# Optimization experiments

Measured on AMD Instinct MI355X. Metric: run time of the kernel, lower is better.

The kernel has to match this reference:

```python
import jax, jax.numpy as jnp
import numpy as np
import math

IN_C = 768
CA = 384
K1 = (3, 1, 1)
K2 = (1, 3, 3)
K3 = (3, 3, 3)


def _dwconv3d(x, w, b):
    # x: [B, Ca, T, H, W]; w: [Ca, 1, kt, kh, kw]; depthwise (groups = Ca)
    pads = [(k // 2, k // 2) for k in w.shape[2:]]
    y = jax.lax.conv_general_dilated(
        x, w, window_strides=(1, 1, 1), padding=pads,
        feature_group_count=x.shape[1],
        dimension_numbers=("NCDHW", "OIDHW", "NCDHW"))
    return y + b[None, :, None, None, None]


def setup_inputs() -> dict:
    key = jax.random.key(0)
    ks = jax.random.split(key, 12)
    s = 0.02
    x = jax.random.normal(ks[0], (128, 197, IN_C), dtype=jnp.float32)
    fc1_w = jax.random.normal(ks[1], (CA, IN_C), dtype=jnp.float32) * s
    fc1_b = jnp.zeros((CA,), dtype=jnp.float32)
    conv1_w = jax.random.normal(ks[2], (CA, 1) + K1, dtype=jnp.float32) * s
    conv1_b = jax.random.normal(ks[3], (CA,), dtype=jnp.float32) * s
    conv2_w = jax.random.normal(ks[4], (CA, 1) + K2, dtype=jnp.float32) * s
    conv2_b = jax.random.normal(ks[5], (CA,), dtype=jnp.float32) * s
    conv3_w = jax.random.normal(ks[6], (CA, 1) + K3, dtype=jnp.float32) * s
    conv3_b = jax.random.normal(ks[7], (CA,), dtype=jnp.float32) * s
    proj_w = jax.random.normal(ks[8], (CA, 1) + K1, dtype=jnp.float32) * s
    proj_b = jax.random.normal(ks[9], (CA,), dtype=jnp.float32) * s
    fc2_w = jax.random.normal(ks[10], (IN_C, CA), dtype=jnp.float32) * s
    fc2_b = jnp.zeros((IN_C,), dtype=jnp.float32)
    return {
        "x": x, "fc1_w": fc1_w, "fc1_b": fc1_b,
        "conv1_w": conv1_w, "conv1_b": conv1_b,
        "conv2_w": conv2_w, "conv2_b": conv2_b,
        "conv3_w": conv3_w, "conv3_b": conv3_b,
        "proj_w": proj_w, "proj_b": proj_b,
        "fc2_w": fc2_w, "fc2_b": fc2_b,
        "T": 16,
    }


def reference(x, fc1_w, fc1_b, conv1_w, conv1_b, conv2_w, conv2_b,
              conv3_w, conv3_b, proj_w, proj_b, fc2_w, fc2_b, T):
    BT, L, C = x.shape
    B = BT // T
    H = W = round(math.sqrt(L - 1))
    Ca = fc1_w.shape[0]
    x_id = x
    # drop CLS token, project down: [BT, L-1, Ca]
    h = jnp.einsum("blc,ac->bla", x[:, 1:, :], fc1_w) + fc1_b
    # [B, Ca, T, H, W]
    h = h.reshape(B, T, H, W, Ca).transpose(0, 4, 1, 2, 3)
    identity = h
    h = (_dwconv3d(h, conv1_w, conv1_b)
         + _dwconv3d(h, conv2_w, conv2_b)
         + _dwconv3d(h, conv3_w, conv3_b)) / 3.0
    h = h + identity
    h = h + _dwconv3d(h, proj_w, proj_b)
    # back to tokens: [BT, L-1, Ca]
    h = h.transpose(0, 2, 3, 4, 1).reshape(BT, L - 1, Ca)
    h = jnp.einsum("bla,ca->blc", h, fc2_w) + fc2_b
    return x_id.at[:, 1:, :].add(h)
```

## Files before the change

### kernel.cpp

```cpp
#include <hip/hip_runtime.h>
#include <cstdint>

typedef __bf16 bf16_t;
typedef __bf16 bf16x8 __attribute__((ext_vector_type(8)));
typedef float f32x4 __attribute__((ext_vector_type(4)));

#define BT_   128
#define LTOK  197
#define CIN   768
#define CA_   384
#define TT    16
#define HH    14
#define NTOK  25088

__device__ __forceinline__ void gl_lds16(const void* g, void* l) {
  __builtin_amdgcn_global_load_lds(
      (const __attribute__((address_space(1))) unsigned int*)g,
      (__attribute__((address_space(3))) unsigned int*)l,
      16, 0, 0);
}

__global__ void prep_weights_kernel(
    const float* __restrict__ c1w, const float* __restrict__ c1b,
    const float* __restrict__ c2w, const float* __restrict__ c2b,
    const float* __restrict__ c3w, const float* __restrict__ c3b,
    const float* __restrict__ projw,
    bf16_t* __restrict__ Wtb,
    float* __restrict__ beff,
    float* __restrict__ pwt) {
  int a = blockIdx.x * blockDim.x + threadIdx.x;
  if (a >= CA_) return;
  for (int dt = 0; dt < 3; dt++)
    for (int dh = 0; dh < 3; dh++)
      for (int dw = 0; dw < 3; dw++) {
        float v = c3w[a*27 + dt*9 + dh*3 + dw];
        if (dh == 1 && dw == 1) v += c1w[a*3 + dt];
        if (dt == 1)            v += c2w[a*9 + dh*3 + dw];
        v *= (1.0f/3.0f);
        if (dt == 1 && dh == 1 && dw == 1) v += 1.0f;
        Wtb[((dt*3+dh)*3+dw)*CA_ + a] = (bf16_t)v;
      }
  beff[a] = (c1b[a] + c2b[a] + c3b[a]) * (1.0f/3.0f);
  pwt[0*CA_ + a] = projw[a*3 + 0];
  pwt[1*CA_ + a] = projw[a*3 + 1];
  pwt[2*CA_ + a] = projw[a*3 + 2];
}

__global__ void convert_w_kernel(const float* __restrict__ fc1w,
                                 const float* __restrict__ fc2w,
                                 const float* __restrict__ x,
                                 float* __restrict__ out,
                                 bf16_t* __restrict__ W1,
                                 bf16_t* __restrict__ W2) {
  int i = blockIdx.x * blockDim.x + threadIdx.x;
  if (i < CA_*CIN) { W1[i] = (bf16_t)fc1w[i]; return; }
  i -= CA_*CIN;
  if (i < CIN*CA_) { W2[i] = (bf16_t)fc2w[i]; return; }
  i -= CIN*CA_;
  if (i < BT_*CIN) {
    int bt = i / CIN, c = i % CIN;
    size_t off = (size_t)bt * LTOK * CIN + c;
    out[off] = x[off];
  }
}

__global__ __launch_bounds__(256) void gemm1_kernel(
    const float* __restrict__ x, const bf16_t* __restrict__ W1,
    const float* __restrict__ fc1b, bf16_t* __restrict__ H0) {
  __shared__ bf16_t Alds[2][128*32];
  __shared__ bf16_t Blds[2][128*32];
  const int tid  = threadIdx.x;
  const int lane = tid & 63;
  const int wave = tid >> 6;
  const int bm = blockIdx.x, bn = blockIdx.y;

  const int arow  = tid >> 1;
  const int kbase = (tid & 1) * 16;
  const int tok   = bm*128 + arow;
  const int bt    = tok / 196;
  const float* xrow = x + (size_t)(tok + bt + 1) * CIN + kbase;
  const int aoff = arow*32 + kbase;

  const bf16_t* bsrc0 = W1 + (size_t)(bn*128 + (tid>>2))*CIN + (tid&3)*8;
  const bf16_t* bsrc1 = bsrc0 + (size_t)64*CIN;
  const int boff0 = tid*8;
  const int boff1 = (tid+256)*8;

  const int quad = lane >> 4;
  const int r16  = lane & 15;
  const int wm = (wave >> 1) * 64;
  const int wn = (wave & 1) * 64;

  f32x4 acc[4][4] = {};

  {
    const float4* xp = (const float4*)xrow;
    float4 f0 = xp[0], f1 = xp[1], f2 = xp[2], f3 = xp[3];
    gl_lds16(bsrc0, &Blds[0][boff0]);
    gl_lds16(bsrc1, &Blds[0][boff1]);
    bf16x8 p0, p1;
    p0[0]=(bf16_t)f0.x; p0[1]=(bf16_t)f0.y; p0[2]=(bf16_t)f0.z; p0[3]=(bf16_t)f0.w;
    p0[4]=(bf16_t)f1.x; p0[5]=(bf16_t)f1.y; p0[6]=(bf16_t)f1.z; p0[7]=(bf16_t)f1.w;
    p1[0]=(bf16_t)f2.x; p1[1]=(bf16_t)f2.y; p1[2]=(bf16_t)f2.z; p1[3]=(bf16_t)f2.w;
    p1[4]=(bf16_t)f3.x; p1[5]=(bf16_t)f3.y; p1[6]=(bf16_t)f3.z; p1[7]=(bf16_t)f3.w;
    *(bf16x8*)&Alds[0][aoff]     = p0;
    *(bf16x8*)&Alds[0][aoff + 8] = p1;
  }
  __syncthreads();

  int cur = 0;
  for (int k0 = 0; k0 < CIN; k0 += 32) {
    const int kn = k0 + 32;
    const bool more = (kn < CIN);
    float4 f0, f1, f2, f3;
    if (more) {
      const float4* xp = (const float4*)(xrow + kn);
      f0 = xp[0]; f1 = xp[1]; f2 = xp[2]; f3 = xp[3];
      gl_lds16(bsrc0 + kn, &Blds[cur^1][boff0]);
      gl_lds16(bsrc1 + kn, &Blds[cur^1][boff1]);
    }

    bf16x8 af[4], bfr[4];
    #pragma unroll
    for (int mt = 0; mt < 4; mt++)
      af[mt] = *(const bf16x8*)&Alds[cur][(wm + mt*16 + r16)*32 + quad*8];
    #pragma unroll
    for (int nt = 0; nt < 4; nt++)
      bfr[nt] = *(const bf16x8*)&Blds[cur][(wn + nt*16 + r16)*32 + quad*8];
    #pragma unroll
    for (int mt = 0; mt < 4; mt++)
      #pragma unroll
      for (int nt = 0; nt < 4; nt++)
        acc[mt][nt] = __builtin_amdgcn_mfma_f32_16x16x32_bf16(af[mt], bfr[nt], acc[mt][nt], 0, 0, 0);

    if (more) {
      bf16x8 p0, p1;
      p0[0]=(bf16_t)f0.x; p0[1]=(bf16_t)f0.y; p0[2]=(bf16_t)f0.z; p0[3]=(bf16_t)f0.w;
      p0[4]=(bf16_t)f1.x; p0[5]=(bf16_t)f1.y; p0[6]=(bf16_t)f1.z; p0[7]=(bf16_t)f1.w;
      p1[0]=(bf16_t)f2.x; p1[1]=(bf16_t)f2.y; p1[2]=(bf16_t)f2.z; p1[3]=(bf16_t)f2.w;
      p1[4]=(bf16_t)f3.x; p1[5]=(bf16_t)f3.y; p1[6]=(bf16_t)f3.z; p1[7]=(bf16_t)f3.w;
      *(bf16x8*)&Alds[cur^1][aoff]     = p0;
      *(bf16x8*)&Alds[cur^1][aoff + 8] = p1;
    }
    __syncthreads();
    cur ^= 1;
  }

  #pragma unroll
  for (int nt = 0; nt < 4; nt++) {
    const int col = bn*128 + wn + nt*16 + r16;
    const float bias = fc1b[col];
    #pragma unroll
    for (int mt = 0; mt < 4; mt++) {
      const int row0 = bm*128 + wm + mt*16 + quad*4;
      #pragma unroll
      for (int rg = 0; rg < 4; rg++)
        H0[(size_t)(row0 + rg)*CA_ + col] = (bf16_t)(acc[mt][nt][rg] + bias);
    }
  }
}

__global__ __launch_bounds__(192) void conv_kernel(
    const bf16_t* __restrict__ H0,
    const bf16_t* __restrict__ Wtb,
    const float* __restrict__ beff,
    const float* __restrict__ pwt,
    const float* __restrict__ pb,
    bf16_t* __restrict__ Z) {
  __shared__ bf16_t Wlds[27*CA_];
  __shared__ float  ybuf[2][2][CA_];

  const int tid = threadIdx.x;
  {
    const uint4* src = (const uint4*)Wtb;
    uint4* dst = (uint4*)Wlds;
    #pragma unroll
    for (int i = 0; i < 7; i++) {
      int idx = tid + i*192;
      if (idx < 27*CA_/8) dst[idx] = src[idx];
    }
  }

  const int blk  = blockIdx.x;
  const int b    = blk & 7;
  const int pair = blk >> 3;
  const int cg   = tid % 48;
  const int ct   = tid / 48;
  const int col  = ct >> 1;
  const int th   = ct & 1;
  const int hw   = pair*2 + col;
  const int h    = hw / HH, w = hw % HH;
  const int c0   = cg * 8;
  const int t0   = th * 8;

  float y[8][8];
  {
    f32x4 bv0 = *(const f32x4*)(beff + c0);
    f32x4 bv1 = *(const f32x4*)(beff + c0 + 4);
    #pragma unroll
    for (int i = 0; i < 8; i++) {
      #pragma unroll
      for (int c = 0; c < 4; c++) { y[i][c] = bv0[c]; y[i][c+4] = bv1[c]; }
    }
  }

  __syncthreads();

  const size_t rowstride = (size_t)196*CA_;
  const bf16_t* base_t0 = H0 + ((size_t)(b*TT + t0)*196)*CA_ + c0;
  const int tau_e_off = th ? -1 : 8;

  for (int j = 0; j < 9; j++) {
    const int dh = j / 3, dw = j - dh*3;
    const int h2 = h + dh - 1, w2 = w + dw - 1;
    const bool ok = ((unsigned)h2 < HH) && ((unsigned)w2 < HH);
    const int sp = ok ? (h2*HH + w2) : hw;
    const float m = ok ? 1.0f : 0.0f;

    const bf16x8 wv0 = *(const bf16x8*)&Wlds[(0*9+j)*CA_ + c0];
    const bf16x8 wv1 = *(const bf16x8*)&Wlds[(1*9+j)*CA_ + c0];
    const bf16x8 wv2 = *(const bf16x8*)&Wlds[(2*9+j)*CA_ + c0];
    float mw0[8], mw1[8], mw2[8];
    #pragma unroll
    for (int c = 0; c < 8; c++) {
      mw0[c] = m * (float)wv0[c];
      mw1[c] = m * (float)wv1[c];
      mw2[c] = m * (float)wv2[c];
    }

    const bf16_t* tp = base_t0 + (size_t)sp*CA_;
    bf16x8 gv[8];
    #pragma unroll
    for (int i = 0; i < 8; i++)
      gv[i] = *(const bf16x8*)(tp + (ptrdiff_t)i*(ptrdiff_t)rowstride);
    const bf16x8 ge = *(const bf16x8*)(tp + (ptrdiff_t)tau_e_off*(ptrdiff_t)rowstride);

    #pragma unroll
    for (int i = 0; i < 8; i++) {
      float gf[8];
      #pragma unroll
      for (int c = 0; c < 8; c++) gf[c] = (float)gv[i][c];
      #pragma unroll
      for (int c = 0; c < 8; c++) y[i][c] += gf[c]*mw1[c];
      if (i > 0) {
        #pragma unroll
        for (int c = 0; c < 8; c++) y[i-1][c] += gf[c]*mw2[c];
      }
      if (i < 7) {
        #pragma unroll
        for (int c = 0; c < 8; c++) y[i+1][c] += gf[c]*mw0[c];
      }
    }
    {
      float gf[8];
      #pragma unroll
      for (int c = 0; c < 8; c++) gf[c] = (float)ge[c];
      if (th) {
        #pragma unroll
        for (int c = 0; c < 8; c++) y[0][c] += gf[c]*mw0[c];
      } else {
        #pragma unroll
        for (int c = 0; c < 8; c++) y[7][c] += gf[c]*mw2[c];
      }
    }
  }

  #pragma unroll
  for (int c = 0; c < 8; c++) ybuf[col][th][c0+c] = th ? y[0][c] : y[7][c];
  __syncthreads();
  float yedge[8];
  #pragma unroll
  for (int c = 0; c < 8; c++) yedge[c] = ybuf[col][1-th][c0+c];

  float p0[8], p1[8], p2[8], pbv[8];
  {
    f32x4 a0 = *(const f32x4*)(pwt + 0*CA_ + c0), a1 = *(const f32x4*)(pwt + 0*CA_ + c0 + 4);
    f32x4 b0 = *(const f32x4*)(pwt + 1*CA_ + c0), b1 = *(const f32x4*)(pwt + 1*CA_ + c0 + 4);
    f32x4 d0 = *(const f32x4*)(pwt + 2*CA_ + c0), d1 = *(const f32x4*)(pwt + 2*CA_ + c0 + 4);
    f32x4 e0 = *(const f32x4*)(pb + c0),          e1 = *(const f32x4*)(pb + c0 + 4);
    #pragma unroll
    for (int c = 0; c < 4; c++) {
      p0[c]=a0[c]; p0[c+4]=a1[c];
      p1[c]=b0[c]; p1[c+4]=b1[c];
      p2[c]=d0[c]; p2[c+4]=d1[c];
      pbv[c]=e0[c]; pbv[c+4]=e1[c];
    }
  }

  bf16_t* zbase = Z + ((size_t)(b*TT + t0)*196 + hw)*CA_ + c0;
  #pragma unroll
  for (int i = 0; i < 8; i++) {
    bf16x8 zo;
    #pragma unroll
    for (int c = 0; c < 8; c++) {
      const float ym = (i > 0) ? y[i-1][c] : (th ? yedge[c] : 0.f);
      const float yp = (i < 7) ? y[i+1][c] : (th ? 0.f : yedge[c]);
      const float z  = y[i][c] + pbv[c] + p0[c]*ym + p1[c]*y[i][c] + p2[c]*yp;
      zo[c] = (bf16_t)z;
    }
    *(bf16x8*)(zbase + (size_t)i*rowstride) = zo;
  }
}

__global__ __launch_bounds__(256) void gemm2_kernel(
    const bf16_t* __restrict__ Z, const bf16_t* __restrict__ W2,
    const float* __restrict__ fc2b, const float* __restrict__ x,
    float* __restrict__ out) {
  __shared__ bf16_t Alds[2][128*32];
  __shared__ bf16_t Blds[2][128*32];
  const int tid  = threadIdx.x;
  const int lane = tid & 63;
  const int wave = tid >> 6;
  const int bm = blockIdx.x, bn = blockIdx.y;

  const bf16_t* asrc0 = Z  + (size_t)(bm*128 + (tid>>2))*CA_ + (tid&3)*8;
  const bf16_t* asrc1 = asrc0 + (size_t)64*CA_;
  const bf16_t* bsrc0 = W2 + (size_t)(bn*128 + (tid>>2))*CA_ + (tid&3)*8;
  const bf16_t* bsrc1 = bsrc0 + (size_t)64*CA_;
  const int aoff0 = tid*8;
  const int aoff1 = (tid+256)*8;

  const int quad = lane >> 4;
  const int r16  = lane & 15;
  const int wm = (wave >> 1) * 64;
  const int wn = (wave & 1) * 64;

  f32x4 acc[4][4] = {};

  gl_lds16(asrc0, &Alds[0][aoff0]);
  gl_lds16(asrc1, &Alds[0][aoff1]);
  gl_lds16(bsrc0, &Blds[0][aoff0]);
  gl_lds16(bsrc1, &Blds[0][aoff1]);
  __syncthreads();

  int cur = 0;
  for (int k0 = 0; k0 < CA_; k0 += 32) {
    const int kn = k0 + 32;
    if (kn < CA_) {
      gl_lds16(asrc0 + kn, &Alds[cur^1][aoff0]);
      gl_lds16(asrc1 + kn, &Alds[cur^1][aoff1]);
      gl_lds16(bsrc0 + kn, &Blds[cur^1][aoff0]);
      gl_lds16(bsrc1 + kn, &Blds[cur^1][aoff1]);
    }
    bf16x8 af[4], bfr[4];
    #pragma unroll
    for (int mt = 0; mt < 4; mt++)
      af[mt] = *(const bf16x8*)&Alds[cur][(wm + mt*16 + r16)*32 + quad*8];
    #pragma unroll
    for (int nt = 0; nt < 4; nt++)
      bfr[nt] = *(const bf16x8*)&Blds[cur][(wn + nt*16 + r16)*32 + quad*8];
    #pragma unroll
    for (int mt = 0; mt < 4; mt++)
      #pragma unroll
      for (int nt = 0; nt < 4; nt++)
        acc[mt][nt] = __builtin_amdgcn_mfma_f32_16x16x32_bf16(af[mt], bfr[nt], acc[mt][nt], 0, 0, 0);
    __syncthreads();
    cur ^= 1;
  }

  #pragma unroll
  for (int nt = 0; nt < 4; nt++) {
    const int col = bn*128 + wn + nt*16 + r16;
    const float bias = fc2b[col];
    #pragma unroll
    for (int mt = 0; mt < 4; mt++) {
      #pragma unroll
      for (int rg = 0; rg < 4; rg++) {
        const int tok = bm*128 + wm + mt*16 + quad*4 + rg;
        const int bt  = tok / 196;
        const size_t o = (size_t)(tok + bt + 1)*CIN + col;
        out[o] = x[o] + acc[mt][nt][rg] + bias;
      }
    }
  }
}

extern "C" void kernel_launch(void* const* d_in, const int* in_sizes, int n_in,
                              void* d_out, int out_size, void* d_ws, size_t ws_size,
                              hipStream_t stream) {
  (void)in_sizes; (void)n_in; (void)out_size; (void)ws_size;
  const float* x    = (const float*)d_in[0];
  const float* fc1w = (const float*)d_in[1];
  const float* fc1b = (const float*)d_in[2];
  const float* c1w  = (const float*)d_in[3];
  const float* c1b  = (const float*)d_in[4];
  const float* c2w  = (const float*)d_in[5];
  const float* c2b  = (const float*)d_in[6];
  const float* c3w  = (const float*)d_in[7];
  const float* c3b  = (const float*)d_in[8];
  const float* pw   = (const float*)d_in[9];
  const float* pb   = (const float*)d_in[10];
  const float* fc2w = (const float*)d_in[11];
  const float* fc2b = (const float*)d_in[12];
  float* out = (float*)d_out;

  char* ws = (char*)d_ws;
  bf16_t* W1   = (bf16_t*)(ws);
  bf16_t* W2   = (bf16_t*)(ws + 589824);
  bf16_t* Wtb  = (bf16_t*)(ws + 1179648);
  float*  beff = (float*) (ws + 1200384);
  float*  pwt  = (float*) (ws + 1201920);
  bf16_t* H0   = (bf16_t*)(ws + 1206528);
  bf16_t* Z    = (bf16_t*)(ws + 20474112);

  prep_weights_kernel<<<dim3(2), dim3(192), 0, stream>>>(
      c1w, c1b, c2w, c2b, c3w, c3b, pw, Wtb, beff, pwt);
  convert_w_kernel<<<dim3(2688), dim3(256), 0, stream>>>(fc1w, fc2w, x, out, W1, W2);
  gemm1_kernel<<<dim3(196, 3), dim3(256), 0, stream>>>(x, W1, fc1b, H0);
  conv_kernel<<<dim3(784), dim3(192), 0, stream>>>(H0, Wtb, beff, pwt, pb, Z);
  gemm2_kernel<<<dim3(196, 6), dim3(256), 0, stream>>>(Z, W2, fc2b, x, out);
}
```

Baseline: 262.4 us.

## Pre-convert activations to bf16 and stream gemm1 A tiles via direct LDS loads

```diff
diff --git a/kernel.cpp b/kernel.cpp
--- a/kernel.cpp
+++ b/kernel.cpp
@@ -2,6 +2,7 @@
 #include <cstdint>
 
 typedef __bf16 bf16_t;
+typedef __bf16 bf16x4 __attribute__((ext_vector_type(4)));
 typedef __bf16 bf16x8 __attribute__((ext_vector_type(8)));
 typedef float f32x4 __attribute__((ext_vector_type(4)));
 
@@ -46,26 +47,44 @@
   pwt[2*CA_ + a] = projw[a*3 + 2];
 }
 
-__global__ void convert_w_kernel(const float* __restrict__ fc1w,
-                                 const float* __restrict__ fc2w,
-                                 const float* __restrict__ x,
-                                 float* __restrict__ out,
-                                 bf16_t* __restrict__ W1,
-                                 bf16_t* __restrict__ W2) {
-  int i = blockIdx.x * blockDim.x + threadIdx.x;
-  if (i < CA_*CIN) { W1[i] = (bf16_t)fc1w[i]; return; }
-  i -= CA_*CIN;
-  if (i < CIN*CA_) { W2[i] = (bf16_t)fc2w[i]; return; }
-  i -= CIN*CA_;
-  if (i < BT_*CIN) {
-    int bt = i / CIN, c = i % CIN;
-    size_t off = (size_t)bt * LTOK * CIN + c;
-    out[off] = x[off];
+__global__ __launch_bounds__(256) void convert_w_kernel(
+    const float* __restrict__ fc1w, const float* __restrict__ fc2w,
+    const float* __restrict__ x, float* __restrict__ out,
+    bf16_t* __restrict__ W1, bf16_t* __restrict__ W2,
+    bf16_t* __restrict__ xb) {
+  const int NW1 = CA_*CIN/4;
+  const int NW2 = CIN*CA_/4;
+  const int NX  = BT_*LTOK*CIN/4;
+  const int total = NW1 + NW2 + NX;
+  for (int i = blockIdx.x*256 + threadIdx.x; i < total; i += gridDim.x*256) {
+    if (i < NW1) {
+      float4 v = ((const float4*)fc1w)[i];
+      bf16x4 b; b[0]=(bf16_t)v.x; b[1]=(bf16_t)v.y; b[2]=(bf16_t)v.z; b[3]=(bf16_t)v.w;
+      *(bf16x4*)(W1 + (size_t)i*4) = b;
+    } else if (i < NW1 + NW2) {
+      int j = i - NW1;
+      float4 v = ((const float4*)fc2w)[j];
+      bf16x4 b; b[0]=(bf16_t)v.x; b[1]=(bf16_t)v.y; b[2]=(bf16_t)v.z; b[3]=(bf16_t)v.w;
+      *(bf16x4*)(W2 + (size_t)j*4) = b;
+    } else {
+      int j = i - NW1 - NW2;
+      int row = j / 192;
+      int c4  = j - row*192;
+      int l   = row % 197;
+      float4 v = ((const float4*)x)[(size_t)j];
+      if (l == 0) {
+        ((float4*)out)[(size_t)j] = v;
+      } else {
+        int tok = (row/197)*196 + (l - 1);
+        bf16x4 b; b[0]=(bf16_t)v.x; b[1]=(bf16_t)v.y; b[2]=(bf16_t)v.z; b[3]=(bf16_t)v.w;
+        *(bf16x4*)(xb + (size_t)tok*CIN + c4*4) = b;
+      }
+    }
   }
 }
 
 __global__ __launch_bounds__(256) void gemm1_kernel(
-    const float* __restrict__ x, const bf16_t* __restrict__ W1,
+    const bf16_t* __restrict__ xb, const bf16_t* __restrict__ W1,
     const float* __restrict__ fc1b, bf16_t* __restrict__ H0) {
   __shared__ bf16_t Alds[2][128*32];
   __shared__ bf16_t Blds[2][128*32];
@@ -74,17 +93,12 @@
   const int wave = tid >> 6;
   const int bm = blockIdx.x, bn = blockIdx.y;
 
-  const int arow  = tid >> 1;
-  const int kbase = (tid & 1) * 16;
-  const int tok   = bm*128 + arow;
-  const int bt    = tok / 196;
-  const float* xrow = x + (size_t)(tok + bt + 1) * CIN + kbase;
-  const int aoff = arow*32 + kbase;
-
+  const bf16_t* asrc0 = xb + (size_t)(bm*128 + (tid>>2))*CIN + (tid&3)*8;
+  const bf16_t* asrc1 = asrc0 + (size_t)64*CIN;
   const bf16_t* bsrc0 = W1 + (size_t)(bn*128 + (tid>>2))*CIN + (tid&3)*8;
   const bf16_t* bsrc1 = bsrc0 + (size_t)64*CIN;
-  const int boff0 = tid*8;
-  const int boff1 = (tid+256)*8;
+  const int aoff0 = tid*8;
+  const int aoff1 = (tid+256)*8;
 
   const int quad = lane >> 4;
   const int r16  = lane & 15;
@@ -93,33 +107,21 @@
 
   f32x4 acc[4][4] = {};
 
-  {
-    const float4* xp = (const float4*)xrow;
-    float4 f0 = xp[0], f1 = xp[1], f2 = xp[2], f3 = xp[3];
-    gl_lds16(bsrc0, &Blds[0][boff0]);
-    gl_lds16(bsrc1, &Blds[0][boff1]);
-    bf16x8 p0, p1;
-    p0[0]=(bf16_t)f0.x; p0[1]=(bf16_t)f0.y; p0[2]=(bf16_t)f0.z; p0[3]=(bf16_t)f0.w;
-    p0[4]=(bf16_t)f1.x; p0[5]=(bf16_t)f1.y; p0[6]=(bf16_t)f1.z; p0[7]=(bf16_t)f1.w;
-    p1[0]=(bf16_t)f2.x; p1[1]=(bf16_t)f2.y; p1[2]=(bf16_t)f2.z; p1[3]=(bf16_t)f2.w;
-    p1[4]=(bf16_t)f3.x; p1[5]=(bf16_t)f3.y; p1[6]=(bf16_t)f3.z; p1[7]=(bf16_t)f3.w;
-    *(bf16x8*)&Alds[0][aoff]     = p0;
-    *(bf16x8*)&Alds[0][aoff + 8] = p1;
-  }
+  gl_lds16(asrc0, &Alds[0][aoff0]);
+  gl_lds16(asrc1, &Alds[0][aoff1]);
+  gl_lds16(bsrc0, &Blds[0][aoff0]);
+  gl_lds16(bsrc1, &Blds[0][aoff1]);
   __syncthreads();
 
   int cur = 0;
   for (int k0 = 0; k0 < CIN; k0 += 32) {
     const int kn = k0 + 32;
-    const bool more = (kn < CIN);
-    float4 f0, f1, f2, f3;
-    if (more) {
-      const float4* xp = (const float4*)(xrow + kn);
-      f0 = xp[0]; f1 = xp[1]; f2 = xp[2]; f3 = xp[3];
-      gl_lds16(bsrc0 + kn, &Blds[cur^1][boff0]);
-      gl_lds16(bsrc1 + kn, &Blds[cur^1][boff1]);
-    }
-
+    if (kn < CIN) {
+      gl_lds16(asrc0 + kn, &Alds[cur^1][aoff0]);
+      gl_lds16(asrc1 + kn, &Alds[cur^1][aoff1]);
+      gl_lds16(bsrc0 + kn, &Blds[cur^1][aoff0]);
+      gl_lds16(bsrc1 + kn, &Blds[cur^1][aoff1]);
+    }
     bf16x8 af[4], bfr[4];
     #pragma unroll
     for (int mt = 0; mt < 4; mt++)
@@ -132,16 +134,6 @@
       #pragma unroll
       for (int nt = 0; nt < 4; nt++)
         acc[mt][nt] = __builtin_amdgcn_mfma_f32_16x16x32_bf16(af[mt], bfr[nt], acc[mt][nt], 0, 0, 0);
-
-    if (more) {
-      bf16x8 p0, p1;
-      p0[0]=(bf16_t)f0.x; p0[1]=(bf16_t)f0.y; p0[2]=(bf16_t)f0.z; p0[3]=(bf16_t)f0.w;
-      p0[4]=(bf16_t)f1.x; p0[5]=(bf16_t)f1.y; p0[6]=(bf16_t)f1.z; p0[7]=(bf16_t)f1.w;
-      p1[0]=(bf16_t)f2.x; p1[1]=(bf16_t)f2.y; p1[2]=(bf16_t)f2.z; p1[3]=(bf16_t)f2.w;
-      p1[4]=(bf16_t)f3.x; p1[5]=(bf16_t)f3.y; p1[6]=(bf16_t)f3.z; p1[7]=(bf16_t)f3.w;
-      *(bf16x8*)&Alds[cur^1][aoff]     = p0;
-      *(bf16x8*)&Alds[cur^1][aoff + 8] = p1;
-    }
     __syncthreads();
     cur ^= 1;
   }
@@ -400,13 +392,14 @@
   bf16_t* Wtb  = (bf16_t*)(ws + 1179648);
   float*  beff = (float*) (ws + 1200384);
   float*  pwt  = (float*) (ws + 1201920);
-  bf16_t* H0   = (bf16_t*)(ws + 1206528);
-  bf16_t* Z    = (bf16_t*)(ws + 20474112);
+  bf16_t* xb   = (bf16_t*)(ws + 1206528);
+  bf16_t* Z    = (bf16_t*)(ws + 1206528);
+  bf16_t* H0   = (bf16_t*)(ws + 39741696);
 
   prep_weights_kernel<<<dim3(2), dim3(192), 0, stream>>>(
       c1w, c1b, c2w, c2b, c3w, c3b, pw, Wtb, beff, pwt);
-  convert_w_kernel<<<dim3(2688), dim3(256), 0, stream>>>(fc1w, fc2w, x, out, W1, W2);
-  gemm1_kernel<<<dim3(196, 3), dim3(256), 0, stream>>>(x, W1, fc1b, H0);
+  convert_w_kernel<<<dim3(4096), dim3(256), 0, stream>>>(fc1w, fc2w, x, out, W1, W2, xb);
+  gemm1_kernel<<<dim3(196, 3), dim3(256), 0, stream>>>(xb, W1, fc1b, H0);
   conv_kernel<<<dim3(784), dim3(192), 0, stream>>>(H0, Wtb, beff, pwt, pb, Z);
   gemm2_kernel<<<dim3(196, 6), dim3(256), 0, stream>>>(Z, W2, fc2b, x, out);
 }
```

After: 266.3 us. About the same (+1.5%).
